# Kernel tuning notes

Hardware: AMD Instinct MI355X
Metric: run time of the kernel (lower is better)

## Reference

```python
import jax, jax.numpy as jnp
import numpy as np

EPS = 1e-10

def _normalized_gradient(x):
    # x: [B, C, H, W]. Central diff in interior, one-sided diff at boundaries.
    g_x = jnp.concatenate([
        x[:, :, 1:2, :] - x[:, :, 0:1, :],       # forward diff at top row
        x[:, :, 2:, :] - x[:, :, :-2, :],        # central diff interior
        x[:, :, -1:, :] - x[:, :, -2:-1, :],     # backward diff at bottom row
    ], axis=2)
    g_y = jnp.concatenate([
        x[:, :, :, 1:2] - x[:, :, :, 0:1],
        x[:, :, :, 2:] - x[:, :, :, :-2],
        x[:, :, :, -1:] - x[:, :, :, -2:-1],
    ], axis=3)
    g = jnp.stack([g_x, g_y], axis=-1)           # [B, C, H, W, 2]
    norm = jnp.sqrt(jnp.sum(g * g, axis=-1, keepdims=True) + EPS)
    return g / norm

def setup_inputs() -> dict:
    key = jax.random.key(0)
    k0, k1 = jax.random.split(key)
    shape = (64, 1, 512, 512)
    I0 = jax.random.normal(k0, shape, dtype=jnp.float32)
    I1 = jax.random.normal(k1, shape, dtype=jnp.float32)
    return {"I0": I0, "I1": I1}

def reference(I0, I1):
    g0 = _normalized_gradient(I0)
    g1 = _normalized_gradient(I1)
    # per-pixel dot product of the two unit gradient vectors
    dot = jnp.sum(g0 * g1, axis=-1)              # [B, C, H, W]
    return 1.0 - jnp.mean(dot * dot)
```

## Files before the change

kernel.cpp:

```cpp
#include <hip/hip_runtime.h>


#define HH 512
#define WW 512
#define NGF_EPS 1e-10f
#define RPT 8

__device__ __forceinline__ float rcp_fast(float x) { return __builtin_amdgcn_rcpf(x); }

__global__ __launch_bounds__(256, 1) void ngf_partial(const float* __restrict__ I0,
                                                      const float* __restrict__ I1,
                                                      float* __restrict__ partials) {
    const int tid  = threadIdx.x;
    const int wv   = tid >> 6;
    const int lane = tid & 63;
    const int gw   = blockIdx.x * 4 + wv;
    const int img  = gw >> 6;
    const int ck   = gw & 63;
    const int h0   = ck * RPT;

    const float* p0 = I0 + (size_t)img * (HH * WW) + lane * 8;
    const float* p1 = I1 + (size_t)img * (HH * WW) + lane * 8;

    float4 u0a, u0b, u1a, u1b, c0a, c0b, c1a, c1b;
    float4 n0a, n0b, n1a, n1b, f0a, f0b, f1a, f1b;
    {
        const int ru = (h0 > 0) ? (h0 - 1) * WW : 0;
        const int rc = h0 * WW;
        const int rn = (h0 + 1) * WW;
        const int rf = (h0 + 2) * WW;
        u0a = *(const float4*)(p0 + ru);     u0b = *(const float4*)(p0 + ru + 4);
        u1a = *(const float4*)(p1 + ru);     u1b = *(const float4*)(p1 + ru + 4);
        c0a = *(const float4*)(p0 + rc);     c0b = *(const float4*)(p0 + rc + 4);
        c1a = *(const float4*)(p1 + rc);     c1b = *(const float4*)(p1 + rc + 4);
        n0a = *(const float4*)(p0 + rn);     n0b = *(const float4*)(p0 + rn + 4);
        n1a = *(const float4*)(p1 + rn);     n1b = *(const float4*)(p1 + rn + 4);
        f0a = *(const float4*)(p0 + rf);     f0b = *(const float4*)(p0 + rf + 4);
        f1a = *(const float4*)(p1 + rf);     f1b = *(const float4*)(p1 + rf + 4);
    }

    float s = 0.f;
#pragma unroll
    for (int i = 0; i < RPT; ++i) {
        const int h  = h0 + i;
        const int hp = (h + 3 < HH) ? h + 3 : HH - 1;
        const int rp = hp * WW;
        const float4 m0a = *(const float4*)(p0 + rp);
        const float4 m0b = *(const float4*)(p0 + rp + 4);
        const float4 m1a = *(const float4*)(p1 + rp);
        const float4 m1b = *(const float4*)(p1 + rp + 4);

        float L0 = __shfl_up(c0b.w, 1, 64);   if (lane == 0)  L0 = c0a.x;
        float R0 = __shfl_down(c0a.x, 1, 64); if (lane == 63) R0 = c0b.w;
        float L1 = __shfl_up(c1b.w, 1, 64);   if (lane == 0)  L1 = c1a.x;
        float R1 = __shfl_down(c1a.x, 1, 64); if (lane == 63) R1 = c1b.w;

        const float a0[10] = {L0, c0a.x, c0a.y, c0a.z, c0a.w,
                                  c0b.x, c0b.y, c0b.z, c0b.w, R0};
        const float a1[10] = {L1, c1a.x, c1a.y, c1a.z, c1a.w,
                                  c1b.x, c1b.y, c1b.z, c1b.w, R1};
        const float gx0[8] = {n0a.x - u0a.x, n0a.y - u0a.y, n0a.z - u0a.z, n0a.w - u0a.w,
                              n0b.x - u0b.x, n0b.y - u0b.y, n0b.z - u0b.z, n0b.w - u0b.w};
        const float gx1[8] = {n1a.x - u1a.x, n1a.y - u1a.y, n1a.z - u1a.z, n1a.w - u1a.w,
                              n1b.x - u1b.x, n1b.y - u1b.y, n1b.z - u1b.z, n1b.w - u1b.w};
#pragma unroll
        for (int j = 0; j < 8; ++j) {
            const float gy0 = a0[j + 2] - a0[j];
            const float gy1 = a1[j + 2] - a1[j];
            const float q0  = gx0[j] * gx0[j] + gy0 * gy0 + NGF_EPS;
            const float q1  = gx1[j] * gx1[j] + gy1 * gy1 + NGF_EPS;
            const float cr  = gx0[j] * gx1[j] + gy0 * gy1;
            s += cr * cr * rcp_fast(q0 * q1);
        }
        u0a = c0a; u0b = c0b; u1a = c1a; u1b = c1b;
        c0a = n0a; c0b = n0b; c1a = n1a; c1b = n1b;
        n0a = f0a; n0b = f0b; n1a = f1a; n1b = f1b;
        f0a = m0a; f0b = m0b; f1a = m1a; f1b = m1b;
    }

#pragma unroll
    for (int off = 32; off > 0; off >>= 1) s += __shfl_down(s, off, 64);
    if (lane == 0) partials[gw] = s;
}

__global__ __launch_bounds__(1024) void ngf_finalize(const float4* __restrict__ partials,
                                                     float inv_n,
                                                     float* __restrict__ out) {
    const float4 v = partials[threadIdx.x];
    float s = v.x + v.y + v.z + v.w;
#pragma unroll
    for (int off = 32; off > 0; off >>= 1) s += __shfl_down(s, off, 64);

    __shared__ float lds[16];
    const int wave = threadIdx.x >> 6;
    const int lane = threadIdx.x & 63;
    if (lane == 0) lds[wave] = s;
    __syncthreads();
    if (threadIdx.x == 0) {
        float tot = 0.f;
#pragma unroll
        for (int i = 0; i < 16; ++i) tot += lds[i];
        out[0] = 1.0f - tot * inv_n;
    }
}

extern "C" void kernel_launch(void* const* d_in, const int* in_sizes, int n_in,
                              void* d_out, int out_size, void* d_ws, size_t ws_size,
                              hipStream_t stream) {
    const float* I0 = (const float*)d_in[0];
    const float* I1 = (const float*)d_in[1];
    float* partials = (float*)d_ws;

    const int N = in_sizes[0];
    ngf_partial<<<1024, 256, 0, stream>>>(I0, I1, partials);
    ngf_finalize<<<1, 1024, 0, stream>>>((const float4*)partials,
                                         1.0f / (float)N, (float*)d_out);
}
```

Before: 145.2 us.

## Issue all tile row loads upfront via inline asm with staged vmcnt waits

For interior chunks, all 10 rows per image are loaded with 40 inline-asm global_load_dwordx4 instructions, using immediate offsets from five base pointers. Each row's compute then waits only on its own data through descending s_waitcnt vmcnt values, so memory latency overlaps the arithmetic. Boundary chunks take a simpler clamped-index path. This raises memory-level parallelism, but it uses many more VGPRs and relies on hand-written waitcnt counts matching the order the loads are issued.

After: 151.4 us. 1.04x slower.

```diff
diff --git a/kernel.cpp b/kernel.cpp
--- a/kernel.cpp
+++ b/kernel.cpp
@@ -6,11 +6,53 @@
 #define NGF_EPS 1e-10f
 #define RPT 8
 
+typedef float vf4 __attribute__((ext_vector_type(4)));
+
 __device__ __forceinline__ float rcp_fast(float x) { return __builtin_amdgcn_rcpf(x); }
 
-__global__ __launch_bounds__(256, 1) void ngf_partial(const float* __restrict__ I0,
-                                                      const float* __restrict__ I1,
-                                                      float* __restrict__ partials) {
+__device__ __forceinline__ float row_contrib(int lane,
+        vf4 u0a, vf4 u0b, vf4 c0a, vf4 c0b, vf4 n0a, vf4 n0b,
+        vf4 u1a, vf4 u1b, vf4 c1a, vf4 c1b, vf4 n1a, vf4 n1b) {
+    float L0 = __shfl_up(c0b.w, 1, 64);   if (lane == 0)  L0 = c0a.x;
+    float R0 = __shfl_down(c0a.x, 1, 64); if (lane == 63) R0 = c0b.w;
+    float L1 = __shfl_up(c1b.w, 1, 64);   if (lane == 0)  L1 = c1a.x;
+    float R1 = __shfl_down(c1a.x, 1, 64); if (lane == 63) R1 = c1b.w;
+
+    const float a0[10] = {L0, c0a.x, c0a.y, c0a.z, c0a.w, c0b.x, c0b.y, c0b.z, c0b.w, R0};
+    const float a1[10] = {L1, c1a.x, c1a.y, c1a.z, c1a.w, c1b.x, c1b.y, c1b.z, c1b.w, R1};
+    const float gx0[8] = {n0a.x - u0a.x, n0a.y - u0a.y, n0a.z - u0a.z, n0a.w - u0a.w,
+                          n0b.x - u0b.x, n0b.y - u0b.y, n0b.z - u0b.z, n0b.w - u0b.w};
+    const float gx1[8] = {n1a.x - u1a.x, n1a.y - u1a.y, n1a.z - u1a.z, n1a.w - u1a.w,
+                          n1b.x - u1b.x, n1b.y - u1b.y, n1b.z - u1b.z, n1b.w - u1b.w};
+    float s = 0.f;
+#pragma unroll
+    for (int j = 0; j < 8; ++j) {
+        const float gy0 = a0[j + 2] - a0[j];
+        const float gy1 = a1[j + 2] - a1[j];
+        const float q0  = gx0[j] * gx0[j] + gy0 * gy0 + NGF_EPS;
+        const float q1  = gx1[j] * gx1[j] + gy1 * gy1 + NGF_EPS;
+        const float cr  = gx0[j] * gx1[j] + gy0 * gy1;
+        s += cr * cr * rcp_fast(q0 * q1);
+    }
+    return s;
+}
+
+#define LD(dst, base, OFF) \
+    asm volatile("global_load_dwordx4 %0, %1, off offset:" #OFF \
+                 : "=v"(dst) : "v"(base))
+#define LDROW(j, b, OA, OB)      \
+    LD(A0a[j], B0[b], OA); LD(A0b[j], B0[b], OB); \
+    LD(A1a[j], B1[b], OA); LD(A1b[j], B1[b], OB)
+#define TIE(j, N) \
+    asm volatile("s_waitcnt vmcnt(" #N ")" \
+                 : "+v"(A0a[j]), "+v"(A0b[j]), "+v"(A1a[j]), "+v"(A1b[j]))
+#define ROWC(i) row_contrib(lane, \
+        A0a[i], A0b[i], A0a[(i)+1], A0b[(i)+1], A0a[(i)+2], A0b[(i)+2], \
+        A1a[i], A1b[i], A1a[(i)+1], A1b[(i)+1], A1a[(i)+2], A1b[(i)+2])
+
+__global__ __launch_bounds__(256, 1) void ngf_partial(const float* I0,
+                                                      const float* I1,
+                                                      float* partials) {
     const int tid  = threadIdx.x;
     const int wv   = tid >> 6;
     const int lane = tid & 63;
@@ -22,60 +64,46 @@
     const float* p0 = I0 + (size_t)img * (HH * WW) + lane * 8;
     const float* p1 = I1 + (size_t)img * (HH * WW) + lane * 8;
 
-    float4 u0a, u0b, u1a, u1b, c0a, c0b, c1a, c1b;
-    float4 n0a, n0b, n1a, n1b, f0a, f0b, f1a, f1b;
-    {
-        const int ru = (h0 > 0) ? (h0 - 1) * WW : 0;
-        const int rc = h0 * WW;
-        const int rn = (h0 + 1) * WW;
-        const int rf = (h0 + 2) * WW;
-        u0a = *(const float4*)(p0 + ru);     u0b = *(const float4*)(p0 + ru + 4);
-        u1a = *(const float4*)(p1 + ru);     u1b = *(const float4*)(p1 + ru + 4);
-        c0a = *(const float4*)(p0 + rc);     c0b = *(const float4*)(p0 + rc + 4);
-        c1a = *(const float4*)(p1 + rc);     c1b = *(const float4*)(p1 + rc + 4);
-        n0a = *(const float4*)(p0 + rn);     n0b = *(const float4*)(p0 + rn + 4);
-        n1a = *(const float4*)(p1 + rn);     n1b = *(const float4*)(p1 + rn + 4);
-        f0a = *(const float4*)(p0 + rf);     f0b = *(const float4*)(p0 + rf + 4);
-        f1a = *(const float4*)(p1 + rf);     f1b = *(const float4*)(p1 + rf + 4);
-    }
+    float s = 0.f;
 
-    float s = 0.f;
+    if (ck != 0 && ck != 63) {
+        uint64_t B0[5], B1[5];
 #pragma unroll
-    for (int i = 0; i < RPT; ++i) {
-        const int h  = h0 + i;
-        const int hp = (h + 3 < HH) ? h + 3 : HH - 1;
-        const int rp = hp * WW;
-        const float4 m0a = *(const float4*)(p0 + rp);
-        const float4 m0b = *(const float4*)(p0 + rp + 4);
-        const float4 m1a = *(const float4*)(p1 + rp);
-        const float4 m1b = *(const float4*)(p1 + rp + 4);
+        for (int b = 0; b < 5; ++b) {
+            B0[b] = (uint64_t)(p0 + (h0 - 1 + 2 * b) * WW);
+            B1[b] = (uint64_t)(p1 + (h0 - 1 + 2 * b) * WW);
+        }
+        vf4 A0a[10], A0b[10], A1a[10], A1b[10];
+        LDROW(0, 0, 0, 16);  LDROW(1, 0, 2048, 2064);
+        LDROW(2, 1, 0, 16);  LDROW(3, 1, 2048, 2064);
+        LDROW(4, 2, 0, 16);  LDROW(5, 2, 2048, 2064);
+        LDROW(6, 3, 0, 16);  LDROW(7, 3, 2048, 2064);
+        LDROW(8, 4, 0, 16);  LDROW(9, 4, 2048, 2064);
 
-        float L0 = __shfl_up(c0b.w, 1, 64);   if (lane == 0)  L0 = c0a.x;
-        float R0 = __shfl_down(c0a.x, 1, 64); if (lane == 63) R0 = c0b.w;
-        float L1 = __shfl_up(c1b.w, 1, 64);   if (lane == 0)  L1 = c1a.x;
-        float R1 = __shfl_down(c1a.x, 1, 64); if (lane == 63) R1 = c1b.w;
-
-        const float a0[10] = {L0, c0a.x, c0a.y, c0a.z, c0a.w,
-                                  c0b.x, c0b.y, c0b.z, c0b.w, R0};
-        const float a1[10] = {L1, c1a.x, c1a.y, c1a.z, c1a.w,
-                                  c1b.x, c1b.y, c1b.z, c1b.w, R1};
-        const float gx0[8] = {n0a.x - u0a.x, n0a.y - u0a.y, n0a.z - u0a.z, n0a.w - u0a.w,
-                              n0b.x - u0b.x, n0b.y - u0b.y, n0b.z - u0b.z, n0b.w - u0b.w};
-        const float gx1[8] = {n1a.x - u1a.x, n1a.y - u1a.y, n1a.z - u1a.z, n1a.w - u1a.w,
-                              n1b.x - u1b.x, n1b.y - u1b.y, n1b.z - u1b.z, n1b.w - u1b.w};
+        TIE(0, 28); TIE(1, 28); TIE(2, 28);
+        s += ROWC(0);
+        TIE(3, 24); s += ROWC(1);
+        TIE(4, 20); s += ROWC(2);
+        TIE(5, 16); s += ROWC(3);
+        TIE(6, 12); s += ROWC(4);
+        TIE(7, 8);  s += ROWC(5);
+        TIE(8, 4);  s += ROWC(6);
+        TIE(9, 0);  s += ROWC(7);
+    } else {
 #pragma unroll
-        for (int j = 0; j < 8; ++j) {
-            const float gy0 = a0[j + 2] - a0[j];
-            const float gy1 = a1[j + 2] - a1[j];
-            const float q0  = gx0[j] * gx0[j] + gy0 * gy0 + NGF_EPS;
-            const float q1  = gx1[j] * gx1[j] + gy1 * gy1 + NGF_EPS;
-            const float cr  = gx0[j] * gx1[j] + gy0 * gy1;
-            s += cr * cr * rcp_fast(q0 * q1);
+        for (int i = 0; i < RPT; ++i) {
+            const int h  = h0 + i;
+            const int hu = (h > 0) ? h - 1 : 0;
+            const int hd = (h < HH - 1) ? h + 1 : HH - 1;
+            const vf4* u0 = (const vf4*)(p0 + hu * WW);
+            const vf4* c0 = (const vf4*)(p0 + h * WW);
+            const vf4* n0 = (const vf4*)(p0 + hd * WW);
+            const vf4* u1 = (const vf4*)(p1 + hu * WW);
+            const vf4* c1 = (const vf4*)(p1 + h * WW);
+            const vf4* n1 = (const vf4*)(p1 + hd * WW);
+            s += row_contrib(lane, u0[0], u0[1], c0[0], c0[1], n0[0], n0[1],
+                                   u1[0], u1[1], c1[0], c1[1], n1[0], n1[1]);
         }
-        u0a = c0a; u0b = c0b; u1a = c1a; u1b = c1b;
-        c0a = n0a; c0b = n0b; c1a = n1a; c1b = n1b;
-        n0a = f0a; n0b = f0b; n1a = f1a; n1b = f1b;
-        f0a = m0a; f0b = m0b; f1a = m1a; f1b = m1b;
     }
 
 #pragma unroll
```
